# Performance work log

Measured on AMD Instinct MI355X. Metric: run time of the kernel, lower is better.

Reference implementation:

```python
import jax, jax.numpy as jnp
import numpy as np

N_NODES = 50000
N_FEAT = 256
N_HID = 256
N_CLASS = 40
N_EDGES = 800000


def setup_inputs() -> dict:
    key = jax.random.key(0)
    ks = jax.random.split(key, 12)
    x = jax.random.normal(ks[0], (N_NODES, N_FEAT), dtype=jnp.float32)
    edge_index = jax.random.randint(ks[1], (2, N_EDGES), 0, N_NODES, dtype=jnp.int64)
    def glorot(k, fan_in, fan_out):
        s = jnp.sqrt(6.0 / (fan_in + fan_out)).astype(jnp.float32)
        return jax.random.uniform(k, (fan_in, fan_out), jnp.float32, -s, s)
    return {
        "x": x,
        "edge_index": edge_index,
        "W1": glorot(ks[2], N_FEAT, N_HID), "b1": jnp.zeros((N_HID,), jnp.float32),
        "W2": glorot(ks[3], N_HID, N_HID), "b2": jnp.zeros((N_HID,), jnp.float32),
        "W3": glorot(ks[4], N_HID, N_HID), "b3": jnp.zeros((N_HID,), jnp.float32),
        "W4": glorot(ks[5], N_HID, N_CLASS), "b4": jnp.zeros((N_CLASS,), jnp.float32),
    }


def _gcn_norm(edge_index, num_nodes):
    # add self-loops, compute symmetric normalization (PyG gcn_norm)
    loop = jnp.arange(num_nodes, dtype=edge_index.dtype)
    src = jnp.concatenate([edge_index[0], loop])
    dst = jnp.concatenate([edge_index[1], loop])
    deg = jax.ops.segment_sum(jnp.ones_like(dst, dtype=jnp.float32), dst,
                              num_segments=num_nodes)
    dis = jnp.where(deg > 0, jax.lax.rsqrt(deg), 0.0)
    norm = dis[src] * dis[dst]  # [E + N]
    return src, dst, norm


def _gcn_conv(x, W, b, src, dst, norm, num_nodes):
    h = x @ W  # dense transform first (out_channels <= in_channels)
    msg = norm[:, None] * h[src]  # gather + scale
    out = jax.ops.segment_sum(msg, dst, num_segments=num_nodes)  # scatter-add
    return out + b


def reference(x, edge_index, W1, b1, W2, b2, W3, b3, W4, b4):
    n = x.shape[0]
    src, dst, norm = _gcn_norm(edge_index, n)
    h = jax.nn.relu(_gcn_conv(x, W1, b1, src, dst, norm, n))
    # dropout is identity in eval mode
    h = jax.nn.relu(_gcn_conv(h, W2, b2, src, dst, norm, n))
    h = jax.nn.relu(_gcn_conv(h, W3, b3, src, dst, norm, n))
    out = _gcn_conv(h, W4, b4, src, dst, norm, n)
    return out
```

## Files before the change

kernel.cpp:

```cpp
#include <hip/hip_runtime.h>

#define NN 50000
#define NF 256
#define NH 256
#define NC 40
#define NE 800000

typedef _Float16 f16x8 __attribute__((ext_vector_type(8)));
typedef float f32x4 __attribute__((ext_vector_type(4)));

__device__ __forceinline__ float f16f(unsigned short u) {
  union { unsigned short u; _Float16 h; } a; a.u = u;
  return (float)a.h;
}
__device__ __forceinline__ unsigned short f16u(float f) {
  union { unsigned short u; _Float16 h; } a; a.h = (_Float16)f;
  return a.u;
}

__device__ __forceinline__ void gl16(const void* g, void* l) {
  __builtin_amdgcn_global_load_lds(
      (const __attribute__((address_space(1))) unsigned int*)g,
      (__attribute__((address_space(3))) unsigned int*)l, 16, 0, 0);
}


__global__ void count_kernel(const int* __restrict__ dst, int* __restrict__ cnt) {
  int e = blockIdx.x * blockDim.x + threadIdx.x;
  if (e < NE) atomicAdd(&cnt[dst[e]], 1);
}

__global__ void dis_kernel(const int* __restrict__ cnt, float* __restrict__ dis) {
  int i = blockIdx.x * blockDim.x + threadIdx.x;
  if (i < NN) dis[i] = rsqrtf((float)(cnt[i] + 1));
}

__global__ __launch_bounds__(1024) void scan1_kernel(const int* __restrict__ cnt,
                                                     int* __restrict__ row_ptr,
                                                     int* __restrict__ bsum) {
  __shared__ int s[1024];
  int i = blockIdx.x * 1024 + threadIdx.x;
  int v = (i < NN) ? cnt[i] : 0;
  s[threadIdx.x] = v;
  __syncthreads();
  for (int ofs = 1; ofs < 1024; ofs <<= 1) {
    int t = (threadIdx.x >= ofs) ? s[threadIdx.x - ofs] : 0;
    __syncthreads();
    s[threadIdx.x] += t;
    __syncthreads();
  }
  if (i < NN) row_ptr[i] = s[threadIdx.x] - v;
  if (threadIdx.x == 1023) bsum[blockIdx.x] = s[1023];
}

__global__ void scan2_kernel(int* __restrict__ bsum) {
  int lane = threadIdx.x;
  const int nb = (NN + 1023) / 1024;
  int v = (lane < nb) ? bsum[lane] : 0;
  for (int ofs = 1; ofs < 64; ofs <<= 1) {
    int t = __shfl_up(v, ofs, 64);
    if (lane >= ofs) v += t;
  }
  if (lane < nb) bsum[lane] = v;
}

__global__ __launch_bounds__(1024) void scan3_kernel(int* __restrict__ row_ptr,
                                                     const int* __restrict__ bsum) {
  int i = blockIdx.x * 1024 + threadIdx.x;
  int add = (blockIdx.x > 0) ? bsum[blockIdx.x - 1] : 0;
  if (i < NN) row_ptr[i] += add;
  if (i == 0) row_ptr[NN] = NE;
}

__global__ void scatter_kernel(const int* __restrict__ src, const int* __restrict__ dst,
                               const int* __restrict__ row_ptr, int* __restrict__ cur,
                               int2* __restrict__ ew, const float* __restrict__ dis) {
  int e = blockIdx.x * blockDim.x + threadIdx.x;
  if (e < NE) {
    int d = dst[e], s = src[e];
    int pos = row_ptr[d] + atomicAdd(&cur[d], 1);
    int2 v; v.x = s; v.y = __float_as_int(dis[s] * dis[d]);
    ew[pos] = v;
  }
}


__global__ __launch_bounds__(256) void xf16_kernel(const float* __restrict__ x,
                                                   unsigned short* __restrict__ P) {
  int i = blockIdx.x * blockDim.x + threadIdx.x;
  if (i >= NN * NF / 4) return;
  float4 v = ((const float4*)x)[i];
  ushort4 h;
  h.x = f16u(v.x); h.y = f16u(v.y); h.z = f16u(v.z); h.w = f16u(v.w);
  ((ushort4*)P)[i] = h;
}

__global__ void wsplit_kernel(const float* __restrict__ W,
                              unsigned short* __restrict__ Whi,
                              unsigned short* __restrict__ Wlo, int N, int NT) {
  int idx = blockIdx.x * blockDim.x + threadIdx.x;
  if (idx >= NT * 256) return;
  int n = idx >> 8, k = idx & 255;
  float v = (n < N) ? W[k * N + n] : 0.0f;
  unsigned short h = f16u(v);
  Whi[idx] = h;
  Wlo[idx] = f16u(v - f16f(h));
}


template <int NSTORE>
__global__ __launch_bounds__(256, 2) void gemm_f16(
    const unsigned short* __restrict__ A,
    const unsigned short* __restrict__ Bthi, const unsigned short* __restrict__ Btlo,
    unsigned short* __restrict__ Cout, int M) {
  __shared__ unsigned short lds[3][128 * 64];

  int tid = threadIdx.x;
  int rowBase = blockIdx.x * 128;
  int colBase = blockIdx.y * 128;
  int w = tid >> 6, lane = tid & 63;
  int wr = w >> 1, wc = w & 1;
  int l15 = lane & 15, l4 = lane >> 4;

  f32x4 acc[4][4] = {};

  for (int kt = 0; kt < 4; ++kt) {
#pragma unroll
    for (int c = 0; c < 4; ++c) {
      int gi = c * 256 + tid;
      int row = gi >> 3, gp = gi & 7;
      int gsrc = gp ^ (row & 7);
      int ar = rowBase + row; ar = ar < M ? ar : M - 1;
      int koff = kt * 64 + gsrc * 8;
      gl16(A + (size_t)ar * 256 + koff, &lds[0][gi * 8]);
      int br = colBase + row;
      gl16(Bthi + (size_t)br * 256 + koff, &lds[1][gi * 8]);
      gl16(Btlo + (size_t)br * 256 + koff, &lds[2][gi * 8]);
    }
    __syncthreads();

#pragma unroll
    for (int ks = 0; ks < 2; ++ks) {
      f16x8 a[4], bh[4], bl[4];
      int g = ks * 4 + l4;
#pragma unroll
      for (int mi = 0; mi < 4; ++mi) {
        int row = wr * 64 + mi * 16 + l15;
        int gp = g ^ (row & 7);
        a[mi] = *(const f16x8*)&lds[0][row * 64 + gp * 8];
      }
#pragma unroll
      for (int ni = 0; ni < 4; ++ni) {
        int row = wc * 64 + ni * 16 + l15;
        int gp = g ^ (row & 7);
        bh[ni] = *(const f16x8*)&lds[1][row * 64 + gp * 8];
        bl[ni] = *(const f16x8*)&lds[2][row * 64 + gp * 8];
      }
#pragma unroll
      for (int mi = 0; mi < 4; ++mi)
#pragma unroll
        for (int ni = 0; ni < 4; ++ni) {
          acc[mi][ni] = __builtin_amdgcn_mfma_f32_16x16x32_f16(a[mi], bh[ni], acc[mi][ni], 0, 0, 0);
          acc[mi][ni] = __builtin_amdgcn_mfma_f32_16x16x32_f16(a[mi], bl[ni], acc[mi][ni], 0, 0, 0);
        }
    }
    __syncthreads();
  }

#pragma unroll
  for (int ni = 0; ni < 4; ++ni) {
    int col = colBase + wc * 64 + ni * 16 + l15;
    if (col < NSTORE) {
#pragma unroll
      for (int mi = 0; mi < 4; ++mi) {
        f32x4 v = acc[mi][ni];
#pragma unroll
        for (int i = 0; i < 4; ++i) {
          int r = rowBase + wr * 64 + mi * 16 + l4 * 4 + i;
          if (r < M) Cout[(size_t)r * NSTORE + col] = f16u(v[i]);
        }
      }
    }
  }
}


__global__ __launch_bounds__(256) void agg256_kernel(
    const unsigned short* __restrict__ T, unsigned short* __restrict__ P,
    const int* __restrict__ rp, const int2* __restrict__ ew,
    const float* __restrict__ dis, const float* __restrict__ b) {
  int node = (blockIdx.x * blockDim.x + threadIdx.x) >> 6;
  int lane = threadIdx.x & 63;
  if (node >= NN) return;
  const ushort4* Tv = (const ushort4*)T;
  float4 bv = ((const float4*)b)[lane];
  float d = dis[node];
  float w0 = d * d;
  ushort4 t = Tv[(size_t)node * 64 + lane];
  float ax = bv.x + w0 * f16f(t.x), ay = bv.y + w0 * f16f(t.y);
  float az = bv.z + w0 * f16f(t.z), aw = bv.w + w0 * f16f(t.w);
  int e = rp[node], end = rp[node + 1];
  for (; e + 4 <= end; e += 4) {
    int2 e0 = ew[e], e1 = ew[e + 1], e2 = ew[e + 2], e3 = ew[e + 3];
    ushort4 t0 = Tv[(size_t)e0.x * 64 + lane];
    ushort4 t1 = Tv[(size_t)e1.x * 64 + lane];
    ushort4 t2 = Tv[(size_t)e2.x * 64 + lane];
    ushort4 t3 = Tv[(size_t)e3.x * 64 + lane];
    float f0 = __int_as_float(e0.y), f1 = __int_as_float(e1.y);
    float f2 = __int_as_float(e2.y), f3 = __int_as_float(e3.y);
    ax += f0 * f16f(t0.x) + f1 * f16f(t1.x) + f2 * f16f(t2.x) + f3 * f16f(t3.x);
    ay += f0 * f16f(t0.y) + f1 * f16f(t1.y) + f2 * f16f(t2.y) + f3 * f16f(t3.y);
    az += f0 * f16f(t0.z) + f1 * f16f(t1.z) + f2 * f16f(t2.z) + f3 * f16f(t3.z);
    aw += f0 * f16f(t0.w) + f1 * f16f(t1.w) + f2 * f16f(t2.w) + f3 * f16f(t3.w);
  }
  for (; e < end; ++e) {
    int2 sw = ew[e];
    float f = __int_as_float(sw.y);
    ushort4 ts = Tv[(size_t)sw.x * 64 + lane];
    ax += f * f16f(ts.x); ay += f * f16f(ts.y);
    az += f * f16f(ts.z); aw += f * f16f(ts.w);
  }
  ax = fmaxf(ax, 0.f); ay = fmaxf(ay, 0.f);
  az = fmaxf(az, 0.f); aw = fmaxf(aw, 0.f);
  ushort4 h;
  h.x = f16u(ax); h.y = f16u(ay); h.z = f16u(az); h.w = f16u(aw);
  ((ushort4*)P)[(size_t)node * 64 + lane] = h;
}

__global__ __launch_bounds__(256) void agg40_kernel(
    const unsigned short* __restrict__ T, float* __restrict__ O,
    const int* __restrict__ rp, const int2* __restrict__ ew,
    const float* __restrict__ dis, const float* __restrict__ b) {
  int node = (blockIdx.x * blockDim.x + threadIdx.x) >> 6;
  int lane = threadIdx.x & 63;
  if (node >= NN) return;
  float d = dis[node];
  int e = rp[node], end = rp[node + 1];
  if (lane < NC) {
    float acc = b[lane] + d * d * f16f(T[(size_t)node * NC + lane]);
    for (; e + 4 <= end; e += 4) {
      int2 e0 = ew[e], e1 = ew[e + 1], e2 = ew[e + 2], e3 = ew[e + 3];
      float t0 = f16f(T[(size_t)e0.x * NC + lane]);
      float t1 = f16f(T[(size_t)e1.x * NC + lane]);
      float t2 = f16f(T[(size_t)e2.x * NC + lane]);
      float t3 = f16f(T[(size_t)e3.x * NC + lane]);
      acc += __int_as_float(e0.y) * t0 + __int_as_float(e1.y) * t1 +
             __int_as_float(e2.y) * t2 + __int_as_float(e3.y) * t3;
    }
    for (; e < end; ++e) {
      int2 sw = ew[e];
      acc += __int_as_float(sw.y) * f16f(T[(size_t)sw.x * NC + lane]);
    }
    O[(size_t)node * NC + lane] = acc;
  }
}


extern "C" void kernel_launch(void* const* d_in, const int* in_sizes, int n_in,
                              void* d_out, int out_size, void* d_ws, size_t ws_size,
                              hipStream_t stream) {
  const float* x  = (const float*)d_in[0];
  const int* edge = (const int*)d_in[1];
  const float* W1 = (const float*)d_in[2];
  const float* b1 = (const float*)d_in[3];
  const float* W2 = (const float*)d_in[4];
  const float* b2 = (const float*)d_in[5];
  const float* W3 = (const float*)d_in[6];
  const float* b3 = (const float*)d_in[7];
  const float* W4 = (const float*)d_in[8];
  const float* b4 = (const float*)d_in[9];
  float* out = (float*)d_out;

  char* p = (char*)d_ws;
  unsigned short* T16 = (unsigned short*)p; p += (size_t)NN * NH * 2;
  unsigned short* P16 = (unsigned short*)p; p += (size_t)NN * NH * 2;
  int* cnt = (int*)p;                p += (size_t)NN * 4;
  float* dis = (float*)p;            p += (size_t)NN * 4;
  int* row_ptr = (int*)p;            p += (size_t)(NN + 16) * 4;
  int* cur = (int*)p;                p += (size_t)NN * 4;
  int* bsum = (int*)p;               p += 256 * 4;
  int2* ew = (int2*)p;               p += (size_t)NE * 8;
  unsigned short* W1thi = (unsigned short*)p; p += 256 * 256 * 2;
  unsigned short* W1tlo = (unsigned short*)p; p += 256 * 256 * 2;
  unsigned short* W2thi = (unsigned short*)p; p += 256 * 256 * 2;
  unsigned short* W2tlo = (unsigned short*)p; p += 256 * 256 * 2;
  unsigned short* W3thi = (unsigned short*)p; p += 256 * 256 * 2;
  unsigned short* W3tlo = (unsigned short*)p; p += 256 * 256 * 2;
  unsigned short* W4thi = (unsigned short*)p; p += 128 * 256 * 2;
  unsigned short* W4tlo = (unsigned short*)p; p += 128 * 256 * 2;

  const int* e_src = edge;
  const int* e_dst = edge + NE;

  hipMemsetAsync(cnt, 0, (size_t)NN * 4, stream);
  hipMemsetAsync(cur, 0, (size_t)NN * 4, stream);

  const int nb1024 = (NN + 1023) / 1024;
  count_kernel<<<(NE + 255) / 256, 256, 0, stream>>>(e_dst, cnt);
  dis_kernel<<<(NN + 255) / 256, 256, 0, stream>>>(cnt, dis);
  scan1_kernel<<<nb1024, 1024, 0, stream>>>(cnt, row_ptr, bsum);
  scan2_kernel<<<1, 64, 0, stream>>>(bsum);
  scan3_kernel<<<nb1024, 1024, 0, stream>>>(row_ptr, bsum);
  scatter_kernel<<<(NE + 255) / 256, 256, 0, stream>>>(e_src, e_dst, row_ptr, cur, ew, dis);

  xf16_kernel<<<(NN * NF / 4 + 255) / 256, 256, 0, stream>>>(x, P16);
  wsplit_kernel<<<256, 256, 0, stream>>>(W1, W1thi, W1tlo, NH, 256);
  wsplit_kernel<<<256, 256, 0, stream>>>(W2, W2thi, W2tlo, NH, 256);
  wsplit_kernel<<<256, 256, 0, stream>>>(W3, W3thi, W3tlo, NH, 256);
  wsplit_kernel<<<128, 256, 0, stream>>>(W4, W4thi, W4tlo, NC, 128);

  dim3 gFull((NN + 127) / 128, 2);
  dim3 gLast((NN + 127) / 128, 1);
  int aggBlocks = (NN * 64 + 255) / 256;

  gemm_f16<256><<<gFull, 256, 0, stream>>>(P16, W1thi, W1tlo, T16, NN);
  agg256_kernel<<<aggBlocks, 256, 0, stream>>>(T16, P16, row_ptr, ew, dis, b1);
  gemm_f16<256><<<gFull, 256, 0, stream>>>(P16, W2thi, W2tlo, T16, NN);
  agg256_kernel<<<aggBlocks, 256, 0, stream>>>(T16, P16, row_ptr, ew, dis, b2);
  gemm_f16<256><<<gFull, 256, 0, stream>>>(P16, W3thi, W3tlo, T16, NN);
  agg256_kernel<<<aggBlocks, 256, 0, stream>>>(T16, P16, row_ptr, ew, dis, b3);
  gemm_f16<NC><<<gLast, 256, 0, stream>>>(P16, W4thi, W4tlo, T16, NN);
  agg40_kernel<<<aggBlocks, 256, 0, stream>>>(T16, out, row_ptr, ew, dis, b4);
}
```

Measured before the change: 409.9 us.

## Drop hi/lo weight split in GEMMs, fuse setup kernels and memsets

Weights are now converted to a single fp16 copy instead of a hi/lo pair, which halves the MFMA count and the B-tile LDS traffic in every GEMM. The degree rsqrt is folded into the first scan kernel, the second and third scan kernels are merged, the four weight-conversion launches become one, and the two memsets become one by placing the counters next to each other. Dropping the low-order weight correction lowers GEMM precision, so accuracy may drift closer to the tolerance.

```diff
diff --git a/kernel.cpp b/kernel.cpp
--- a/kernel.cpp
+++ b/kernel.cpp
@@ -30,17 +30,14 @@
   if (e < NE) atomicAdd(&cnt[dst[e]], 1);
 }
 
-__global__ void dis_kernel(const int* __restrict__ cnt, float* __restrict__ dis) {
-  int i = blockIdx.x * blockDim.x + threadIdx.x;
-  if (i < NN) dis[i] = rsqrtf((float)(cnt[i] + 1));
-}
-
 __global__ __launch_bounds__(1024) void scan1_kernel(const int* __restrict__ cnt,
                                                      int* __restrict__ row_ptr,
-                                                     int* __restrict__ bsum) {
+                                                     int* __restrict__ bsum,
+                                                     float* __restrict__ dis) {
   __shared__ int s[1024];
   int i = blockIdx.x * 1024 + threadIdx.x;
   int v = (i < NN) ? cnt[i] : 0;
+  if (i < NN) dis[i] = rsqrtf((float)(v + 1));
   s[threadIdx.x] = v;
   __syncthreads();
   for (int ofs = 1; ofs < 1024; ofs <<= 1) {
@@ -53,21 +50,22 @@
   if (threadIdx.x == 1023) bsum[blockIdx.x] = s[1023];
 }
 
-__global__ void scan2_kernel(int* __restrict__ bsum) {
-  int lane = threadIdx.x;
+__global__ __launch_bounds__(1024) void scan23_kernel(int* __restrict__ row_ptr,
+                                                      const int* __restrict__ bsum) {
+  __shared__ int sb[64];
   const int nb = (NN + 1023) / 1024;
-  int v = (lane < nb) ? bsum[lane] : 0;
-  for (int ofs = 1; ofs < 64; ofs <<= 1) {
-    int t = __shfl_up(v, ofs, 64);
-    if (lane >= ofs) v += t;
-  }
-  if (lane < nb) bsum[lane] = v;
-}
-
-__global__ __launch_bounds__(1024) void scan3_kernel(int* __restrict__ row_ptr,
-                                                     const int* __restrict__ bsum) {
+  if (threadIdx.x < 64) {
+    int lane = threadIdx.x;
+    int v = (lane < nb) ? bsum[lane] : 0;
+    for (int ofs = 1; ofs < 64; ofs <<= 1) {
+      int t = __shfl_up(v, ofs, 64);
+      if (lane >= ofs) v += t;
+    }
+    sb[lane] = v;
+  }
+  __syncthreads();
   int i = blockIdx.x * 1024 + threadIdx.x;
-  int add = (blockIdx.x > 0) ? bsum[blockIdx.x - 1] : 0;
+  int add = (blockIdx.x > 0) ? sb[blockIdx.x - 1] : 0;
   if (i < NN) row_ptr[i] += add;
   if (i == 0) row_ptr[NN] = NE;
 }
@@ -95,25 +93,28 @@
   ((ushort4*)P)[i] = h;
 }
 
-__global__ void wsplit_kernel(const float* __restrict__ W,
-                              unsigned short* __restrict__ Whi,
-                              unsigned short* __restrict__ Wlo, int N, int NT) {
+__global__ void wf16_kernel(const float* __restrict__ W1, const float* __restrict__ W2,
+                            const float* __restrict__ W3, const float* __restrict__ W4,
+                            unsigned short* __restrict__ Wt1, unsigned short* __restrict__ Wt2,
+                            unsigned short* __restrict__ Wt3, unsigned short* __restrict__ Wt4) {
   int idx = blockIdx.x * blockDim.x + threadIdx.x;
-  if (idx >= NT * 256) return;
+  const float* W; unsigned short* Wt; int N;
+  if (idx < 65536)       { W = W1; Wt = Wt1; N = 256; }
+  else if (idx < 131072) { W = W2; Wt = Wt2; N = 256; idx -= 65536; }
+  else if (idx < 196608) { W = W3; Wt = Wt3; N = 256; idx -= 131072; }
+  else if (idx < 229376) { W = W4; Wt = Wt4; N = 40;  idx -= 196608; }
+  else return;
   int n = idx >> 8, k = idx & 255;
   float v = (n < N) ? W[k * N + n] : 0.0f;
-  unsigned short h = f16u(v);
-  Whi[idx] = h;
-  Wlo[idx] = f16u(v - f16f(h));
+  Wt[idx] = f16u(v);
 }
 
 
 template <int NSTORE>
 __global__ __launch_bounds__(256, 2) void gemm_f16(
-    const unsigned short* __restrict__ A,
-    const unsigned short* __restrict__ Bthi, const unsigned short* __restrict__ Btlo,
+    const unsigned short* __restrict__ A, const unsigned short* __restrict__ Bt,
     unsigned short* __restrict__ Cout, int M) {
-  __shared__ unsigned short lds[3][128 * 64];
+  __shared__ unsigned short lds[2][128 * 64];
 
   int tid = threadIdx.x;
   int rowBase = blockIdx.x * 128;
@@ -134,14 +135,13 @@
       int koff = kt * 64 + gsrc * 8;
       gl16(A + (size_t)ar * 256 + koff, &lds[0][gi * 8]);
       int br = colBase + row;
-      gl16(Bthi + (size_t)br * 256 + koff, &lds[1][gi * 8]);
-      gl16(Btlo + (size_t)br * 256 + koff, &lds[2][gi * 8]);
+      gl16(Bt + (size_t)br * 256 + koff, &lds[1][gi * 8]);
     }
     __syncthreads();
 
 #pragma unroll
     for (int ks = 0; ks < 2; ++ks) {
-      f16x8 a[4], bh[4], bl[4];
+      f16x8 a[4], b[4];
       int g = ks * 4 + l4;
 #pragma unroll
       for (int mi = 0; mi < 4; ++mi) {
@@ -153,16 +153,13 @@
       for (int ni = 0; ni < 4; ++ni) {
         int row = wc * 64 + ni * 16 + l15;
         int gp = g ^ (row & 7);
-        bh[ni] = *(const f16x8*)&lds[1][row * 64 + gp * 8];
-        bl[ni] = *(const f16x8*)&lds[2][row * 64 + gp * 8];
+        b[ni] = *(const f16x8*)&lds[1][row * 64 + gp * 8];
       }
 #pragma unroll
       for (int mi = 0; mi < 4; ++mi)
 #pragma unroll
-        for (int ni = 0; ni < 4; ++ni) {
-          acc[mi][ni] = __builtin_amdgcn_mfma_f32_16x16x32_f16(a[mi], bh[ni], acc[mi][ni], 0, 0, 0);
-          acc[mi][ni] = __builtin_amdgcn_mfma_f32_16x16x32_f16(a[mi], bl[ni], acc[mi][ni], 0, 0, 0);
-        }
+        for (int ni = 0; ni < 4; ++ni)
+          acc[mi][ni] = __builtin_amdgcn_mfma_f32_16x16x32_f16(a[mi], b[ni], acc[mi][ni], 0, 0, 0);
     }
     __syncthreads();
   }
@@ -275,50 +272,40 @@
   unsigned short* T16 = (unsigned short*)p; p += (size_t)NN * NH * 2;
   unsigned short* P16 = (unsigned short*)p; p += (size_t)NN * NH * 2;
   int* cnt = (int*)p;                p += (size_t)NN * 4;
+  int* cur = (int*)p;                p += (size_t)NN * 4;
   float* dis = (float*)p;            p += (size_t)NN * 4;
   int* row_ptr = (int*)p;            p += (size_t)(NN + 16) * 4;
-  int* cur = (int*)p;                p += (size_t)NN * 4;
   int* bsum = (int*)p;               p += 256 * 4;
   int2* ew = (int2*)p;               p += (size_t)NE * 8;
-  unsigned short* W1thi = (unsigned short*)p; p += 256 * 256 * 2;
-  unsigned short* W1tlo = (unsigned short*)p; p += 256 * 256 * 2;
-  unsigned short* W2thi = (unsigned short*)p; p += 256 * 256 * 2;
-  unsigned short* W2tlo = (unsigned short*)p; p += 256 * 256 * 2;
-  unsigned short* W3thi = (unsigned short*)p; p += 256 * 256 * 2;
-  unsigned short* W3tlo = (unsigned short*)p; p += 256 * 256 * 2;
-  unsigned short* W4thi = (unsigned short*)p; p += 128 * 256 * 2;
-  unsigned short* W4tlo = (unsigned short*)p; p += 128 * 256 * 2;
+  unsigned short* Wt1 = (unsigned short*)p; p += 256 * 256 * 2;
+  unsigned short* Wt2 = (unsigned short*)p; p += 256 * 256 * 2;
+  unsigned short* Wt3 = (unsigned short*)p; p += 256 * 256 * 2;
+  unsigned short* Wt4 = (unsigned short*)p; p += 128 * 256 * 2;
 
   const int* e_src = edge;
   const int* e_dst = edge + NE;
 
-  hipMemsetAsync(cnt, 0, (size_t)NN * 4, stream);
-  hipMemsetAsync(cur, 0, (size_t)NN * 4, stream);
+  hipMemsetAsync(cnt, 0, (size_t)NN * 8, stream);
 
   const int nb1024 = (NN + 1023) / 1024;
   count_kernel<<<(NE + 255) / 256, 256, 0, stream>>>(e_dst, cnt);
-  dis_kernel<<<(NN + 255) / 256, 256, 0, stream>>>(cnt, dis);
-  scan1_kernel<<<nb1024, 1024, 0, stream>>>(cnt, row_ptr, bsum);
-  scan2_kernel<<<1, 64, 0, stream>>>(bsum);
-  scan3_kernel<<<nb1024, 1024, 0, stream>>>(row_ptr, bsum);
+  scan1_kernel<<<nb1024, 1024, 0, stream>>>(cnt, row_ptr, bsum, dis);
+  scan23_kernel<<<nb1024, 1024, 0, stream>>>(row_ptr, bsum);
   scatter_kernel<<<(NE + 255) / 256, 256, 0, stream>>>(e_src, e_dst, row_ptr, cur, ew, dis);
 
   xf16_kernel<<<(NN * NF / 4 + 255) / 256, 256, 0, stream>>>(x, P16);
-  wsplit_kernel<<<256, 256, 0, stream>>>(W1, W1thi, W1tlo, NH, 256);
-  wsplit_kernel<<<256, 256, 0, stream>>>(W2, W2thi, W2tlo, NH, 256);
-  wsplit_kernel<<<256, 256, 0, stream>>>(W3, W3thi, W3tlo, NH, 256);
-  wsplit_kernel<<<128, 256, 0, stream>>>(W4, W4thi, W4tlo, NC, 128);
+  wf16_kernel<<<(229376 + 255) / 256, 256, 0, stream>>>(W1, W2, W3, W4, Wt1, Wt2, Wt3, Wt4);
 
   dim3 gFull((NN + 127) / 128, 2);
   dim3 gLast((NN + 127) / 128, 1);
   int aggBlocks = (NN * 64 + 255) / 256;
 
-  gemm_f16<256><<<gFull, 256, 0, stream>>>(P16, W1thi, W1tlo, T16, NN);
+  gemm_f16<256><<<gFull, 256, 0, stream>>>(P16, Wt1, T16, NN);
   agg256_kernel<<<aggBlocks, 256, 0, stream>>>(T16, P16, row_ptr, ew, dis, b1);
-  gemm_f16<256><<<gFull, 256, 0, stream>>>(P16, W2thi, W2tlo, T16, NN);
+  gemm_f16<256><<<gFull, 256, 0, stream>>>(P16, Wt2, T16, NN);
   agg256_kernel<<<aggBlocks, 256, 0, stream>>>(T16, P16, row_ptr, ew, dis, b2);
-  gemm_f16<256><<<gFull, 256, 0, stream>>>(P16, W3thi, W3tlo, T16, NN);
+  gemm_f16<256><<<gFull, 256, 0, stream>>>(P16, Wt3, T16, NN);
   agg256_kernel<<<aggBlocks, 256, 0, stream>>>(T16, P16, row_ptr, ew, dis, b3);
-  gemm_f16<NC><<<gLast, 256, 0, stream>>>(P16, W4thi, W4tlo, T16, NN);
+  gemm_f16<NC><<<gLast, 256, 0, stream>>>(P16, Wt4, T16, NN);
   agg40_kernel<<<aggBlocks, 256, 0, stream>>>(T16, out, row_ptr, ew, dis, b4);
 }
```

Result: faster. 381.9 us (-6.8%).
